# Kernel tuning notes

Measured on AMD Instinct MI355X. Metric: run time of the kernel, lower is better.

Reference implementation:

```python
import jax, jax.numpy as jnp
import numpy as np

B, T, F_DIM = 32, 512, 128
HID, OUT, KS = 256, 4, 3
PAD_LEN = 512          # round(T * (200/stage_timepoints - 1)), stage_timepoints = 100
MMD_SIGMA = 1.0
DILATIONS = (1, 2, 4)  # config.dilation_expand = 2, num_layers = 3


def setup_inputs() -> dict:
    key = jax.random.key(0)
    keys = iter(jax.random.split(key, 40))
    s = 0.05

    def lin(o, i):
        return jax.random.normal(next(keys), (o, i), jnp.float32) * s

    def vec(o):
        return jnp.zeros((o,), jnp.float32)

    inp = {
        "feature1": jax.random.normal(next(keys), (B, F_DIM, 1, T), jnp.float32),
        "feature2": jax.random.normal(next(keys), (B, F_DIM, 1, T), jnp.float32),
    }
    # cross-attention params (A and B branches)
    for tag in ("a", "b"):
        for nm in ("q", "k", "v"):
            inp["w%s_%s" % (nm, tag)] = lin(F_DIM, F_DIM)
            inp["b%s_%s" % (nm, tag)] = vec(F_DIM)
    # TCN layers
    in_ch = F_DIM
    for i in range(3):
        inp["conv_w%d" % i] = jax.random.normal(next(keys), (HID, in_ch, KS), jnp.float32) * s
        inp["conv_b%d" % i] = vec(HID)
        inp["res_w%d" % i] = lin(HID, in_ch)
        inp["res_b%d" % i] = vec(HID)
        in_ch = HID
    inp["fc_w"] = lin(OUT, HID)
    inp["fc_b"] = vec(OUT)
    return inp


def _cross_attention(A, Bseq, wq, bq, wk, bk, wv, bv):
    # A, Bseq: [B, T, F]
    Q = A @ wq.T + bq
    K = Bseq @ wk.T + bk
    V = Bseq @ wv.T + bv
    scale = 1.0 / jnp.sqrt(jnp.asarray(Q.shape[-1], Q.dtype))
    scores = jnp.einsum('btf,bsf->bts', Q, K) * scale
    w = jax.nn.softmax(scores, axis=-1)
    return jnp.einsum('bts,bsf->btf', w, V)


def _tcn_layer(x, cw, cb, rw, rb, dilation):
    # x: [B, C, T]; causal left pad then dilated conv
    pad = (KS - 1) * dilation
    xp = jnp.pad(x, ((0, 0), (0, 0), (pad, 0)))
    out = jax.lax.conv_general_dilated(
        xp, cw, window_strides=(1,), padding='VALID',
        rhs_dilation=(dilation,), dimension_numbers=('NCH', 'OIH', 'NCH'))
    out = jax.nn.relu(out + cb[None, :, None])
    res = jnp.einsum('bct,oc->bot', x, rw) + rb[None, :, None]
    return out + res


def _pairwise_dist(x, y):
    # x, y: [B, T, F] -> [B, B, T]; ||x_i - y_j||^2 per time point via norm expansion
    sx = jnp.sum(x * x, axis=-1)  # [B, T]
    sy = jnp.sum(y * y, axis=-1)  # [B, T]
    return sx[:, None, :] + sy[None, :, :] - 2.0 * jnp.einsum('itf,jtf->ijt', x, y)


def _mmd_loss(f1, f2):
    inv = 1.0 / (2.0 * MMD_SIGMA ** 2)
    K_XX = jnp.exp(-_pairwise_dist(f1, f1) * inv)
    K_YY = jnp.exp(-_pairwise_dist(f2, f2) * inv)
    K_XY = jnp.exp(-_pairwise_dist(f1, f2) * inv)
    return jnp.mean(K_XX + K_YY - 2.0 * K_XY)


def reference(feature1, feature2,
              wq_a, bq_a, wk_a, bk_a, wv_a, bv_a,
              wq_b, bq_b, wk_b, bk_b, wv_b, bv_b,
              conv_w0, conv_b0, res_w0, res_b0,
              conv_w1, conv_b1, res_w1, res_b1,
              conv_w2, conv_b2, res_w2, res_b2,
              fc_w, fc_b):
    # [B, F, 1, T] -> [B, T, F]
    f1 = jnp.transpose(feature1[:, :, 0, :], (0, 2, 1))
    f2 = jnp.transpose(feature2[:, :, 0, :], (0, 2, 1))

    f1 = _cross_attention(f2, f1, wq_a, bq_a, wk_a, bk_a, wv_a, bv_a) * f1 + f1
    f2 = _cross_attention(f1, f2, wq_b, bq_b, wk_b, bk_b, wv_b, bv_b) * f2 + f2

    # temporal-offset padding: f1 padded right, f2 padded left, then summed
    p1 = jnp.pad(f1, ((0, 0), (0, PAD_LEN), (0, 0)))
    p2 = jnp.pad(f2, ((0, 0), (PAD_LEN, 0), (0, 0)))
    x = jnp.transpose(p1 + p2, (0, 2, 1))  # [B, F, T+PAD]

    tcn_params = ((conv_w0, conv_b0, res_w0, res_b0),
                  (conv_w1, conv_b1, res_w1, res_b1),
                  (conv_w2, conv_b2, res_w2, res_b2))
    for (cw, cb, rw, rb), d in zip(tcn_params, DILATIONS):
        x = _tcn_layer(x, cw, cb, rw, rb, d)

    pooled = jnp.mean(x, axis=2)          # [B, HID]
    output = pooled @ fc_w.T + fc_b       # [B, OUT]
    loss = _mmd_loss(f1, f2)
    return output, loss
```

## Files before the change

kernel.cpp:

```cpp
#include <hip/hip_runtime.h>

#define BB 32
#define TT 512
#define FF 128
#define HID 256
#define TP 1024

typedef __attribute__((ext_vector_type(8))) short s16x8;
typedef __attribute__((ext_vector_type(8))) unsigned short u16x8;
typedef __attribute__((ext_vector_type(4))) unsigned short u16x4;
typedef __attribute__((ext_vector_type(4))) float f32x4;

static __device__ __forceinline__ unsigned short f2bf(float f) {
    unsigned u = __builtin_bit_cast(unsigned, f);
    u = (u + 0x7FFFu + ((u >> 16) & 1u)) >> 16;
    return (unsigned short)u;
}
static __device__ __forceinline__ float bf2f(unsigned short b) {
    return __builtin_bit_cast(float, ((unsigned)b) << 16);
}

__global__ __launch_bounds__(256) void t2bf_kernel(
    const float* __restrict__ src1, const float* __restrict__ src2,
    unsigned short* __restrict__ dst1, unsigned short* __restrict__ dst2)
{
    int t0 = blockIdx.x * 32, c0 = blockIdx.y * 32;
    int sel = blockIdx.z >> 5, b = blockIdx.z & 31;
    const float* src = sel ? src2 : src1;
    unsigned short* dst = sel ? dst2 : dst1;
    __shared__ float tile[32][33];
    int tid = threadIdx.x;
    for (int l = tid; l < 1024; l += 256) {
        int c = l >> 5, t = l & 31;
        tile[c][t] = src[((size_t)b * FF + c0 + c) * TT + t0 + t];
    }
    __syncthreads();
    for (int l = tid; l < 1024; l += 256) {
        int t = l >> 5, c = l & 31;
        dst[((size_t)b * TT + t0 + t) * FF + c0 + c] = f2bf(tile[c][t]);
    }
}

static __device__ __forceinline__ void tcnw_prep(
    int idx, const float* __restrict__ cw, const float* __restrict__ rw,
    unsigned short* __restrict__ out, int Cin)
{
    int p = idx / (256 * Cin);
    int rem = idx - p * 256 * Cin;
    int o = rem / Cin, c = rem - o * Cin;
    float v = (p < 3) ? cw[(o * Cin + c) * 3 + p] : rw[o * Cin + c];
    out[idx] = f2bf(v);
}

__global__ __launch_bounds__(256) void prep_all_kernel(
    const float* __restrict__ wqa, const float* __restrict__ wka,
    const float* __restrict__ wva, const float* __restrict__ wqb,
    const float* __restrict__ wkb, const float* __restrict__ wvb,
    const float* __restrict__ cw0, const float* __restrict__ rw0,
    const float* __restrict__ cw1, const float* __restrict__ rw1,
    const float* __restrict__ cw2, const float* __restrict__ rw2,
    unsigned short* __restrict__ qkvw, unsigned short* __restrict__ wb0,
    unsigned short* __restrict__ wb1, unsigned short* __restrict__ wb2)
{
    int idx = blockIdx.x * 256 + threadIdx.x;
    if (idx < 98304) {
        int p = idx >> 14, rc = idx & 16383;
        const float* srcs[6] = {wqa, wka, wva, wqb, wkb, wvb};
        float v = srcs[p][rc];
        if (p == 0 || p == 3) v *= 0.088388347648318447f;
        qkvw[idx] = f2bf(v);
    } else if (idx < 229376) {
        tcnw_prep(idx - 98304, cw0, rw0, wb0, 128);
    } else if (idx < 491520) {
        tcnw_prep(idx - 229376, cw1, rw1, wb1, 256);
    } else if (idx < 753664) {
        tcnw_prep(idx - 491520, cw2, rw2, wb2, 256);
    }
}

__global__ __launch_bounds__(256) void proj_mfma_kernel(
    const unsigned short* __restrict__ xq_src, long long xq_bs,
    const unsigned short* __restrict__ xkv_src, long long xkv_bs,
    const unsigned short* __restrict__ w3,
    const float* __restrict__ bq, const float* __restrict__ bk,
    const float* __restrict__ bv,
    unsigned short* __restrict__ Qo, unsigned short* __restrict__ Ko,
    unsigned short* __restrict__ Vt)
{
    int t0 = blockIdx.x * 32, b = blockIdx.y;
    __shared__ __align__(16) unsigned short xsq[32 * 136];
    __shared__ __align__(16) unsigned short xskv[32 * 136];
    int tid = threadIdx.x;
    int wid = tid >> 6, lane = tid & 63;
    int n = lane & 15, g = lane >> 4;
    int tsub = (wid & 1) * 16, fh = (wid >> 1) * 64;

    for (int l = tid; l < 512; l += 256) {
        int r = l >> 4, cc = l & 15;
        *(u16x8*)&xsq[r * 136 + cc * 8] =
            *(const u16x8*)&xq_src[xq_bs * b + (size_t)(t0 + r) * FF + cc * 8];
        *(u16x8*)&xskv[r * 136 + cc * 8] =
            *(const u16x8*)&xkv_src[xkv_bs * b + (size_t)(t0 + r) * FF + cc * 8];
    }
    __syncthreads();

    f32x4 acc[3][4];
#pragma unroll
    for (int p = 0; p < 3; ++p)
#pragma unroll
        for (int i = 0; i < 4; ++i) acc[p][i] = (f32x4){0.f, 0.f, 0.f, 0.f};

#pragma unroll
    for (int kk = 0; kk < 4; ++kk) {
        s16x8 bxq = *(const s16x8*)&xsq[(tsub + n) * 136 + kk * 32 + g * 8];
        s16x8 bxkv = *(const s16x8*)&xskv[(tsub + n) * 136 + kk * 32 + g * 8];
#pragma unroll
        for (int i = 0; i < 4; ++i) {
            const unsigned short* wb = &w3[(size_t)(fh + i * 16 + n) * 128 + kk * 32 + g * 8];
            s16x8 a0 = *(const s16x8*)&wb[0];
            s16x8 a1 = *(const s16x8*)&wb[16384];
            s16x8 a2 = *(const s16x8*)&wb[32768];
            acc[0][i] = __builtin_amdgcn_mfma_f32_16x16x32_bf16(a0, bxq, acc[0][i], 0, 0, 0);
            acc[1][i] = __builtin_amdgcn_mfma_f32_16x16x32_bf16(a1, bxkv, acc[1][i], 0, 0, 0);
            acc[2][i] = __builtin_amdgcn_mfma_f32_16x16x32_bf16(a2, bxkv, acc[2][i], 0, 0, 0);
        }
    }

    const float scale = 0.088388347648318447f;
    int t = t0 + tsub + n;
#pragma unroll
    for (int i = 0; i < 4; ++i) {
        int fb = fh + i * 16 + g * 4;
        u16x4 pk;
#pragma unroll
        for (int r = 0; r < 4; ++r) pk[r] = f2bf(acc[0][i][r] + bq[fb + r] * scale);
        *(u16x4*)&Qo[((size_t)b * TT + t) * FF + fb] = pk;
#pragma unroll
        for (int r = 0; r < 4; ++r) pk[r] = f2bf(acc[1][i][r] + bk[fb + r]);
        *(u16x4*)&Ko[((size_t)b * TT + t) * FF + fb] = pk;
#pragma unroll
        for (int r = 0; r < 4; ++r)
            Vt[((size_t)b * FF + fb + r) * TT + t] = f2bf(acc[2][i][r] + bv[fb + r]);
    }
}

__global__ __launch_bounds__(256) void attn_mfma_kernel(
    const unsigned short* __restrict__ Qb, const unsigned short* __restrict__ Kb,
    const unsigned short* __restrict__ Vtb,
    const float* __restrict__ orig, long long bso, int cso, int tso,
    float* __restrict__ out_tf, unsigned short* __restrict__ out_x, int xoff)
{
    __shared__ __align__(16) unsigned short Ks[64 * 136];
    __shared__ __align__(16) unsigned short Vs[128 * 72];
    __shared__ __align__(16) unsigned short Ps[4 * 16 * 68];

    int t0 = blockIdx.x * 64, b = blockIdx.y;
    int tid = threadIdx.x;
    int wid = tid >> 6, lane = tid & 63;
    int n = lane & 15, g = lane >> 4;
    int q0 = t0 + wid * 16;
    unsigned short* Pw = &Ps[wid * 1088];

    s16x8 qf[4];
#pragma unroll
    for (int kk = 0; kk < 4; ++kk)
        qf[kk] = *(const s16x8*)&Qb[((size_t)b * TT + q0 + n) * FF + kk * 32 + g * 8];

    u16x8 kst[4], vst[4];
#pragma unroll
    for (int ii = 0; ii < 4; ++ii) {
        int l = tid + 256 * ii;
        kst[ii] = *(const u16x8*)&Kb[((size_t)b * TT + (l >> 4)) * FF + (l & 15) * 8];
        vst[ii] = *(const u16x8*)&Vtb[((size_t)b * FF + (l >> 3)) * TT + (l & 7) * 8];
    }

    f32x4 O[8];
#pragma unroll
    for (int ft = 0; ft < 8; ++ft) O[ft] = (f32x4){0.f, 0.f, 0.f, 0.f};
    float m[4] = {-1e30f, -1e30f, -1e30f, -1e30f};
    float lsum[4] = {0.f, 0.f, 0.f, 0.f};

    for (int it = 0; it < 8; ++it) {
        __syncthreads();
#pragma unroll
        for (int ii = 0; ii < 4; ++ii) {
            int l = tid + 256 * ii;
            *(u16x8*)&Ks[(l >> 4) * 136 + (l & 15) * 8] = kst[ii];
            *(u16x8*)&Vs[(l >> 3) * 72 + (l & 7) * 8] = vst[ii];
        }
        __syncthreads();
        if (it < 7) {
            int s0n = (it + 1) * 64;
#pragma unroll
            for (int ii = 0; ii < 4; ++ii) {
                int l = tid + 256 * ii;
                kst[ii] = *(const u16x8*)&Kb[((size_t)b * TT + s0n + (l >> 4)) * FF + (l & 15) * 8];
                vst[ii] = *(const u16x8*)&Vtb[((size_t)b * FF + (l >> 3)) * TT + s0n + (l & 7) * 8];
            }
        }

        f32x4 acc[4];
#pragma unroll
        for (int st = 0; st < 4; ++st) acc[st] = (f32x4){0.f, 0.f, 0.f, 0.f};
#pragma unroll
        for (int kk = 0; kk < 4; ++kk) {
#pragma unroll
            for (int st = 0; st < 4; ++st) {
                s16x8 kf = *(const s16x8*)&Ks[(st * 16 + n) * 136 + kk * 32 + g * 8];
                acc[st] = __builtin_amdgcn_mfma_f32_16x16x32_bf16(qf[kk], kf, acc[st], 0, 0, 0);
            }
        }

        float mnew[4], c[4], rs[4];
#pragma unroll
        for (int r = 0; r < 4; ++r) {
            float tm = fmaxf(fmaxf(acc[0][r], acc[1][r]), fmaxf(acc[2][r], acc[3][r]));
#pragma unroll
            for (int msk = 1; msk < 16; msk <<= 1) tm = fmaxf(tm, __shfl_xor(tm, msk));
            mnew[r] = fmaxf(m[r], tm);
            c[r] = __expf(m[r] - mnew[r]);
            m[r] = mnew[r];
            rs[r] = 0.f;
        }
#pragma unroll
        for (int st = 0; st < 4; ++st) {
#pragma unroll
            for (int r = 0; r < 4; ++r) {
                float p = __expf(acc[st][r] - mnew[r]);
                rs[r] += p;
                Pw[(g * 4 + r) * 68 + st * 16 + n] = f2bf(p);
            }
        }
#pragma unroll
        for (int r = 0; r < 4; ++r) {
#pragma unroll
            for (int msk = 1; msk < 16; msk <<= 1) rs[r] += __shfl_xor(rs[r], msk);
            lsum[r] = lsum[r] * c[r] + rs[r];
        }
#pragma unroll
        for (int ft = 0; ft < 8; ++ft) {
#pragma unroll
            for (int r = 0; r < 4; ++r) O[ft][r] *= c[r];
        }

#pragma unroll
        for (int ks = 0; ks < 2; ++ks) {
            s16x8 pf = *(const s16x8*)&Pw[n * 68 + ks * 32 + g * 8];
#pragma unroll
            for (int ft = 0; ft < 8; ++ft) {
                s16x8 vf = *(const s16x8*)&Vs[(ft * 16 + n) * 72 + ks * 32 + g * 8];
                O[ft] = __builtin_amdgcn_mfma_f32_16x16x32_bf16(pf, vf, O[ft], 0, 0, 0);
            }
        }
    }

    float rinv[4];
#pragma unroll
    for (int r = 0; r < 4; ++r) rinv[r] = 1.f / lsum[r];
#pragma unroll
    for (int ft = 0; ft < 8; ++ft) {
        int f = ft * 16 + n;
#pragma unroll
        for (int r = 0; r < 4; ++r) {
            int q = q0 + g * 4 + r;
            float val = O[ft][r] * rinv[r];
            float xv = orig[bso * b + (size_t)f * cso + (size_t)q * tso];
            float res = val * xv + xv;
            out_tf[((size_t)b * TT + q) * FF + f] = res;
            out_x[((size_t)b * TP + xoff + q) * FF + f] = f2bf(res);
        }
    }
}

__global__ __launch_bounds__(256) void mmd_kernel(
    const float* __restrict__ f1, const float* __restrict__ f2,
    float* __restrict__ partials)
{
    int t = blockIdx.x;
    __shared__ float v1[32][129], v2[32][129];
    __shared__ float red[256];
    int tid = threadIdx.x;
    for (int l = tid; l < 4096; l += 256) {
        int i = l >> 7, f = l & 127;
        v1[i][f] = f1[((size_t)i * TT + t) * FF + f];
        v2[i][f] = f2[((size_t)i * TT + t) * FF + f];
    }
    __syncthreads();
    float s = 0.f;
    for (int r = 0; r < 4; ++r) {
        int p = tid + 256 * r;
        int i = p >> 5, j = p & 31;
        float dxx = 0.f, dyy = 0.f, dxy = 0.f;
        for (int f = 0; f < 128; ++f) {
            float a = v1[i][f], b_ = v1[j][f], c = v2[i][f], d = v2[j][f];
            float e1 = a - b_, e2 = c - d, e3 = a - d;
            dxx += e1 * e1; dyy += e2 * e2; dxy += e3 * e3;
        }
        s += __expf(-0.5f * dxx) + __expf(-0.5f * dyy) - 2.f * __expf(-0.5f * dxy);
    }
    red[tid] = s;
    __syncthreads();
    for (int off = 128; off; off >>= 1) {
        if (tid < off) red[tid] += red[tid + off];
        __syncthreads();
    }
    if (tid == 0) partials[t] = red[0];
}

__global__ __launch_bounds__(256, 2) void tcn_mfma_kernel(
    const unsigned short* __restrict__ x, int Cin, int d,
    const unsigned short* __restrict__ w4,
    const float* __restrict__ cb, const float* __restrict__ rb,
    unsigned short* __restrict__ out, float* __restrict__ pool_out, int do_pool)
{
    int t0 = blockIdx.x * 256, o0 = blockIdx.y * 64, b = blockIdx.z;
    __shared__ __align__(16) unsigned short xs[264 * 40];
    __shared__ __align__(16) unsigned short wsh[4 * 64 * 40];
    __shared__ float pool_s[4][64];
    int tid = threadIdx.x;
    int wid = tid >> 6, lane = tid & 63;
    int n = lane & 15, g = lane >> 4;
    int wt = wid * 64;
    int d2 = 2 * d;
    int nrow = 256 + d2;
    const unsigned short* xb = x + (size_t)b * TP * Cin;

    int gg = tid & 3;
    int xr0 = tid >> 2;
    int tg0 = t0 - d2 + xr0;
    bool xv4 = xr0 < d2;
    const unsigned short* wbase = w4 + (size_t)(o0 + (tid >> 2)) * Cin + gg * 8;
    size_t wps = (size_t)256 * Cin;

    u16x8 sx0, sx1, sx2, sx3, sx4, sw0, sw1, sw2, sw3;
    const u16x8 zz = {0, 0, 0, 0, 0, 0, 0, 0};
#define LDST(C0)                                                               \
    do {                                                                       \
        sx0 = (tg0 >= 0) ? *(const u16x8*)&xb[(size_t)tg0 * Cin + (C0) + gg * 8] : zz; \
        sx1 = *(const u16x8*)&xb[(size_t)(tg0 + 64) * Cin + (C0) + gg * 8];    \
        sx2 = *(const u16x8*)&xb[(size_t)(tg0 + 128) * Cin + (C0) + gg * 8];   \
        sx3 = *(const u16x8*)&xb[(size_t)(tg0 + 192) * Cin + (C0) + gg * 8];   \
        sx4 = xv4 ? *(const u16x8*)&xb[(size_t)(tg0 + 256) * Cin + (C0) + gg * 8] : zz; \
        sw0 = *(const u16x8*)&wbase[(C0)];                                     \
        sw1 = *(const u16x8*)&wbase[wps + (C0)];                               \
        sw2 = *(const u16x8*)&wbase[2 * wps + (C0)];                           \
        sw3 = *(const u16x8*)&wbase[3 * wps + (C0)];                           \
    } while (0)

    f32x4 accc[4][4], accr[4][4];
#pragma unroll
    for (int i = 0; i < 4; ++i)
#pragma unroll
        for (int j = 0; j < 4; ++j) {
            accc[i][j] = (f32x4){0.f, 0.f, 0.f, 0.f};
            accr[i][j] = (f32x4){0.f, 0.f, 0.f, 0.f};
        }

    LDST(0);
    for (int c0 = 0; c0 < Cin; c0 += 32) {
        __syncthreads();
        *(u16x8*)&xs[xr0 * 40 + gg * 8] = sx0;
        *(u16x8*)&xs[(xr0 + 64) * 40 + gg * 8] = sx1;
        *(u16x8*)&xs[(xr0 + 128) * 40 + gg * 8] = sx2;
        *(u16x8*)&xs[(xr0 + 192) * 40 + gg * 8] = sx3;
        if (xv4) *(u16x8*)&xs[(xr0 + 256) * 40 + gg * 8] = sx4;
        {
            int wrow = (tid >> 2) * 40 + gg * 8;
            *(u16x8*)&wsh[wrow] = sw0;
            *(u16x8*)&wsh[2560 + wrow] = sw1;
            *(u16x8*)&wsh[5120 + wrow] = sw2;
            *(u16x8*)&wsh[7680 + wrow] = sw3;
        }
        __syncthreads();
        if (c0 + 32 < Cin) LDST(c0 + 32);

        s16x8 bfr[4][3];
#pragma unroll
        for (int j = 0; j < 4; ++j) {
            int tl = wt + j * 16 + n;
#pragma unroll
            for (int k = 0; k < 3; ++k)
                bfr[j][k] = *(const s16x8*)&xs[(tl + k * d) * 40 + g * 8];
        }
#pragma unroll
        for (int i = 0; i < 4; ++i) {
            int wrow = (i * 16 + n) * 40 + g * 8;
            s16x8 a0 = *(const s16x8*)&wsh[wrow];
            s16x8 a1 = *(const s16x8*)&wsh[2560 + wrow];
            s16x8 a2 = *(const s16x8*)&wsh[5120 + wrow];
            s16x8 ar = *(const s16x8*)&wsh[7680 + wrow];
#pragma unroll
            for (int j = 0; j < 4; ++j) {
                accc[i][j] = __builtin_amdgcn_mfma_f32_16x16x32_bf16(a0, bfr[j][0], accc[i][j], 0, 0, 0);
                accc[i][j] = __builtin_amdgcn_mfma_f32_16x16x32_bf16(a1, bfr[j][1], accc[i][j], 0, 0, 0);
                accc[i][j] = __builtin_amdgcn_mfma_f32_16x16x32_bf16(a2, bfr[j][2], accc[i][j], 0, 0, 0);
                accr[i][j] = __builtin_amdgcn_mfma_f32_16x16x32_bf16(ar, bfr[j][2], accr[i][j], 0, 0, 0);
            }
        }
    }
#undef LDST

#pragma unroll
    for (int i = 0; i < 4; ++i) {
        int ob = o0 + i * 16 + g * 4;
        float cbv0 = cb[ob], cbv1 = cb[ob + 1], cbv2 = cb[ob + 2], cbv3 = cb[ob + 3];
        float rbv0 = rb[ob], rbv1 = rb[ob + 1], rbv2 = rb[ob + 2], rbv3 = rb[ob + 3];
        float ps0 = 0.f, ps1 = 0.f, ps2 = 0.f, ps3 = 0.f;
#pragma unroll
        for (int j = 0; j < 4; ++j) {
            int t = t0 + wt + j * 16 + n;
            float v0 = fmaxf(accc[i][j][0] + cbv0, 0.f) + accr[i][j][0] + rbv0;
            float v1 = fmaxf(accc[i][j][1] + cbv1, 0.f) + accr[i][j][1] + rbv1;
            float v2 = fmaxf(accc[i][j][2] + cbv2, 0.f) + accr[i][j][2] + rbv2;
            float v3 = fmaxf(accc[i][j][3] + cbv3, 0.f) + accr[i][j][3] + rbv3;
            ps0 += v0; ps1 += v1; ps2 += v2; ps3 += v3;
            if (!do_pool) {
                u16x4 pk;
                pk[0] = f2bf(v0); pk[1] = f2bf(v1); pk[2] = f2bf(v2); pk[3] = f2bf(v3);
                *(u16x4*)&out[((size_t)b * TP + t) * HID + ob] = pk;
            }
        }
        if (do_pool) {
#pragma unroll
            for (int msk = 1; msk < 16; msk <<= 1) {
                ps0 += __shfl_xor(ps0, msk);
                ps1 += __shfl_xor(ps1, msk);
                ps2 += __shfl_xor(ps2, msk);
                ps3 += __shfl_xor(ps3, msk);
            }
            if (n == 0) {
                int ol = i * 16 + g * 4;
                pool_s[wid][ol + 0] = ps0;
                pool_s[wid][ol + 1] = ps1;
                pool_s[wid][ol + 2] = ps2;
                pool_s[wid][ol + 3] = ps3;
            }
        }
    }
    if (do_pool) {
        __syncthreads();
        if (tid < 64) {
            float s = pool_s[0][tid] + pool_s[1][tid] + pool_s[2][tid] + pool_s[3][tid];
            pool_out[((size_t)b * 4 + blockIdx.x) * HID + o0 + tid] = s;
        }
    }
}

__global__ __launch_bounds__(256) void final_kernel(
    const float* __restrict__ pp, const float* __restrict__ fcw,
    const float* __restrict__ fcb, const float* __restrict__ partials,
    float* __restrict__ dout)
{
    int tid = threadIdx.x;
    if (tid < 128) {
        int b = tid >> 2, k = tid & 3;
        float s = 0.f;
        for (int c = 0; c < HID; ++c) {
            float pc = 0.f;
#pragma unroll
            for (int xs = 0; xs < 4; ++xs) pc += pp[((size_t)b * 4 + xs) * HID + c];
            s += pc * fcw[k * HID + c];
        }
        dout[tid] = fcb[k] + s * (1.f / 1024.f);
    } else if (tid < 192) {
        int lane = tid - 128;
        float s = 0.f;
        for (int j = 0; j < 8; ++j) s += partials[lane + 64 * j];
        for (int off = 32; off; off >>= 1) s += __shfl_down(s, off);
        if (lane == 0) dout[128] = s * (1.f / (32.f * 32.f * 512.f));
    }
}

extern "C" void kernel_launch(void* const* d_in, const int* in_sizes, int n_in,
                              void* d_out, int out_size, void* d_ws, size_t ws_size,
                              hipStream_t stream)
{
    const float* feat1 = (const float*)d_in[0];
    const float* feat2 = (const float*)d_in[1];
    const float* wq_a = (const float*)d_in[2];
    const float* bq_a = (const float*)d_in[3];
    const float* wk_a = (const float*)d_in[4];
    const float* bk_a = (const float*)d_in[5];
    const float* wv_a = (const float*)d_in[6];
    const float* bv_a = (const float*)d_in[7];
    const float* wq_b = (const float*)d_in[8];
    const float* bq_b = (const float*)d_in[9];
    const float* wk_b = (const float*)d_in[10];
    const float* bk_b = (const float*)d_in[11];
    const float* wv_b = (const float*)d_in[12];
    const float* bv_b = (const float*)d_in[13];
    const float* cw0 = (const float*)d_in[14];
    const float* cb0 = (const float*)d_in[15];
    const float* rw0 = (const float*)d_in[16];
    const float* rb0 = (const float*)d_in[17];
    const float* cw1 = (const float*)d_in[18];
    const float* cb1 = (const float*)d_in[19];
    const float* rw1 = (const float*)d_in[20];
    const float* rb1 = (const float*)d_in[21];
    const float* cw2 = (const float*)d_in[22];
    const float* cb2 = (const float*)d_in[23];
    const float* rw2 = (const float*)d_in[24];
    const float* rb2 = (const float*)d_in[25];
    const float* fcw = (const float*)d_in[26];
    const float* fcb = (const float*)d_in[27];
    float* dout = (float*)d_out;

    float* ws = (float*)d_ws;
    unsigned short* Qbf = (unsigned short*)ws;
    unsigned short* Kbf = (unsigned short*)(ws + 1048576);
    unsigned short* Vt  = (unsigned short*)(ws + 2097152);
    float* f1tf = ws + 3145728;
    float* f2tf = ws + 5242880;
    unsigned short* xbuf = (unsigned short*)(ws + 7340032);
    unsigned short* wbuf = (unsigned short*)(ws + 9437184);
    unsigned short* wb0 = wbuf;
    unsigned short* wb1 = wbuf + 131072;
    unsigned short* wb2 = wbuf + 393216;
    unsigned short* xbf1 = (unsigned short*)(ws + 9798144);
    unsigned short* xbf2 = (unsigned short*)(ws + 10846720);
    unsigned short* qkvw = (unsigned short*)(ws + 11895296);
    unsigned short* w3a = qkvw;
    unsigned short* w3b = qkvw + 3 * 16384;
    float* poolpart = ws + 11944448;
    float* mmdpart  = ws + 11977216;
    unsigned short* h_a = (unsigned short*)ws;
    unsigned short* h_b = (unsigned short*)(ws + 4194304);

    t2bf_kernel<<<dim3(16, 4, 64), 256, 0, stream>>>(feat1, feat2, xbf1, xbf2);
    prep_all_kernel<<<dim3(2944), 256, 0, stream>>>(
        wq_a, wk_a, wv_a, wq_b, wk_b, wv_b,
        cw0, rw0, cw1, rw1, cw2, rw2, qkvw, wb0, wb1, wb2);

    proj_mfma_kernel<<<dim3(16, 32), 256, 0, stream>>>(
        xbf2, (long long)TT * FF, xbf1, (long long)TT * FF, w3a,
        bq_a, bk_a, bv_a, Qbf, Kbf, Vt);
    attn_mfma_kernel<<<dim3(8, 32), 256, 0, stream>>>(
        Qbf, Kbf, Vt, feat1, 65536LL, 512, 1, f1tf, xbuf, 0);

    proj_mfma_kernel<<<dim3(16, 32), 256, 0, stream>>>(
        xbuf, (long long)TP * FF, xbf2, (long long)TT * FF, w3b,
        bq_b, bk_b, bv_b, Qbf, Kbf, Vt);
    attn_mfma_kernel<<<dim3(8, 32), 256, 0, stream>>>(
        Qbf, Kbf, Vt, feat2, 65536LL, 512, 1, f2tf, xbuf, 512);

    mmd_kernel<<<dim3(512), 256, 0, stream>>>(f1tf, f2tf, mmdpart);

    tcn_mfma_kernel<<<dim3(4, 4, 32), 256, 0, stream>>>(xbuf, 128, 1, wb0, cb0, rb0, h_a, nullptr, 0);
    tcn_mfma_kernel<<<dim3(4, 4, 32), 256, 0, stream>>>(h_a, 256, 2, wb1, cb1, rb1, h_b, nullptr, 0);
    tcn_mfma_kernel<<<dim3(4, 4, 32), 256, 0, stream>>>(h_b, 256, 4, wb2, cb2, rb2, h_a, poolpart, 1);

    final_kernel<<<dim3(1), 256, 0, stream>>>(poolpart, fcw, fcb, mmdpart, dout);
}
```

Measured before the change: 198.5 us.

## Fuse input transpose into projection, MFMA-based MMD Gram, attention priority hints

```diff
diff --git a/kernel.cpp b/kernel.cpp
--- a/kernel.cpp
+++ b/kernel.cpp
@@ -18,27 +18,6 @@
 }
 static __device__ __forceinline__ float bf2f(unsigned short b) {
     return __builtin_bit_cast(float, ((unsigned)b) << 16);
-}
-
-__global__ __launch_bounds__(256) void t2bf_kernel(
-    const float* __restrict__ src1, const float* __restrict__ src2,
-    unsigned short* __restrict__ dst1, unsigned short* __restrict__ dst2)
-{
-    int t0 = blockIdx.x * 32, c0 = blockIdx.y * 32;
-    int sel = blockIdx.z >> 5, b = blockIdx.z & 31;
-    const float* src = sel ? src2 : src1;
-    unsigned short* dst = sel ? dst2 : dst1;
-    __shared__ float tile[32][33];
-    int tid = threadIdx.x;
-    for (int l = tid; l < 1024; l += 256) {
-        int c = l >> 5, t = l & 31;
-        tile[c][t] = src[((size_t)b * FF + c0 + c) * TT + t0 + t];
-    }
-    __syncthreads();
-    for (int l = tid; l < 1024; l += 256) {
-        int t = l >> 5, c = l & 31;
-        dst[((size_t)b * TT + t0 + t) * FF + c0 + c] = f2bf(tile[c][t]);
-    }
 }
 
 static __device__ __forceinline__ void tcnw_prep(
@@ -79,8 +58,8 @@
 }
 
 __global__ __launch_bounds__(256) void proj_mfma_kernel(
-    const unsigned short* __restrict__ xq_src, long long xq_bs,
-    const unsigned short* __restrict__ xkv_src, long long xkv_bs,
+    const void* __restrict__ xq_src, int xq_mode, long long xq_bs,
+    const void* __restrict__ xkv_src, int xkv_mode, long long xkv_bs,
     const unsigned short* __restrict__ w3,
     const float* __restrict__ bq, const float* __restrict__ bk,
     const float* __restrict__ bv,
@@ -95,12 +74,31 @@
     int n = lane & 15, g = lane >> 4;
     int tsub = (wid & 1) * 16, fh = (wid >> 1) * 64;
 
-    for (int l = tid; l < 512; l += 256) {
-        int r = l >> 4, cc = l & 15;
-        *(u16x8*)&xsq[r * 136 + cc * 8] =
-            *(const u16x8*)&xq_src[xq_bs * b + (size_t)(t0 + r) * FF + cc * 8];
-        *(u16x8*)&xskv[r * 136 + cc * 8] =
-            *(const u16x8*)&xkv_src[xkv_bs * b + (size_t)(t0 + r) * FF + cc * 8];
+    if (xq_mode == 0) {
+        const float* s = (const float*)xq_src + (size_t)b * xq_bs;
+        for (int l = tid; l < 4096; l += 256) {
+            int c = l >> 5, tt = l & 31;
+            xsq[tt * 136 + c] = f2bf(s[(size_t)c * TT + t0 + tt]);
+        }
+    } else {
+        const unsigned short* s = (const unsigned short*)xq_src + (size_t)b * xq_bs;
+        for (int l = tid; l < 512; l += 256) {
+            int r = l >> 4, cc = l & 15;
+            *(u16x8*)&xsq[r * 136 + cc * 8] = *(const u16x8*)&s[(size_t)(t0 + r) * FF + cc * 8];
+        }
+    }
+    if (xkv_mode == 0) {
+        const float* s = (const float*)xkv_src + (size_t)b * xkv_bs;
+        for (int l = tid; l < 4096; l += 256) {
+            int c = l >> 5, tt = l & 31;
+            xskv[tt * 136 + c] = f2bf(s[(size_t)c * TT + t0 + tt]);
+        }
+    } else {
+        const unsigned short* s = (const unsigned short*)xkv_src + (size_t)b * xkv_bs;
+        for (int l = tid; l < 512; l += 256) {
+            int r = l >> 4, cc = l & 15;
+            *(u16x8*)&xskv[r * 136 + cc * 8] = *(const u16x8*)&s[(size_t)(t0 + r) * FF + cc * 8];
+        }
     }
     __syncthreads();
 
@@ -202,6 +200,7 @@
         f32x4 acc[4];
 #pragma unroll
         for (int st = 0; st < 4; ++st) acc[st] = (f32x4){0.f, 0.f, 0.f, 0.f};
+        __builtin_amdgcn_s_setprio(1);
 #pragma unroll
         for (int kk = 0; kk < 4; ++kk) {
 #pragma unroll
@@ -210,6 +209,7 @@
                 acc[st] = __builtin_amdgcn_mfma_f32_16x16x32_bf16(qf[kk], kf, acc[st], 0, 0, 0);
             }
         }
+        __builtin_amdgcn_s_setprio(0);
 
         float mnew[4], c[4], rs[4];
 #pragma unroll
@@ -243,6 +243,7 @@
             for (int r = 0; r < 4; ++r) O[ft][r] *= c[r];
         }
 
+        __builtin_amdgcn_s_setprio(1);
 #pragma unroll
         for (int ks = 0; ks < 2; ++ks) {
             s16x8 pf = *(const s16x8*)&Pw[n * 68 + ks * 32 + g * 8];
@@ -252,6 +253,7 @@
                 O[ft] = __builtin_amdgcn_mfma_f32_16x16x32_bf16(pf, vf, O[ft], 0, 0, 0);
             }
         }
+        __builtin_amdgcn_s_setprio(0);
     }
 
     float rinv[4];
@@ -277,26 +279,64 @@
     float* __restrict__ partials)
 {
     int t = blockIdx.x;
-    __shared__ float v1[32][129], v2[32][129];
+    __shared__ __align__(16) unsigned short X1h[32 * 136], X1l[32 * 136];
+    __shared__ __align__(16) unsigned short X2h[32 * 136], X2l[32 * 136];
+    __shared__ float Gs[3][32][33];
     __shared__ float red[256];
     int tid = threadIdx.x;
+
     for (int l = tid; l < 4096; l += 256) {
         int i = l >> 7, f = l & 127;
-        v1[i][f] = f1[((size_t)i * TT + t) * FF + f];
-        v2[i][f] = f2[((size_t)i * TT + t) * FF + f];
+        float v1 = f1[((size_t)i * TT + t) * FF + f];
+        float v2 = f2[((size_t)i * TT + t) * FF + f];
+        unsigned short h1 = f2bf(v1);
+        unsigned short h2 = f2bf(v2);
+        X1h[i * 136 + f] = h1;
+        X1l[i * 136 + f] = f2bf(v1 - bf2f(h1));
+        X2h[i * 136 + f] = h2;
+        X2l[i * 136 + f] = f2bf(v2 - bf2f(h2));
     }
     __syncthreads();
+
+    int wid = tid >> 6, lane = tid & 63;
+    int n = lane & 15, g = lane >> 4;
+#pragma unroll
+    for (int uu = 0; uu < 3; ++uu) {
+        int u = wid * 3 + uu;
+        int gram = u >> 2, quad = u & 3;
+        int qi = quad >> 1, qj = quad & 1;
+        const unsigned short* Ah = (gram == 1) ? X2h : X1h;
+        const unsigned short* Al = (gram == 1) ? X2l : X1l;
+        const unsigned short* Bh = (gram == 0) ? X1h : X2h;
+        const unsigned short* Bl = (gram == 0) ? X1l : X2l;
+        f32x4 acc = (f32x4){0.f, 0.f, 0.f, 0.f};
+#pragma unroll
+        for (int kk = 0; kk < 4; ++kk) {
+            int ao = (qi * 16 + n) * 136 + kk * 32 + g * 8;
+            int bo = (qj * 16 + n) * 136 + kk * 32 + g * 8;
+            s16x8 ah = *(const s16x8*)&Ah[ao];
+            s16x8 al = *(const s16x8*)&Al[ao];
+            s16x8 bh = *(const s16x8*)&Bh[bo];
+            s16x8 bl = *(const s16x8*)&Bl[bo];
+            acc = __builtin_amdgcn_mfma_f32_16x16x32_bf16(ah, bh, acc, 0, 0, 0);
+            acc = __builtin_amdgcn_mfma_f32_16x16x32_bf16(ah, bl, acc, 0, 0, 0);
+            acc = __builtin_amdgcn_mfma_f32_16x16x32_bf16(al, bh, acc, 0, 0, 0);
+        }
+#pragma unroll
+        for (int r = 0; r < 4; ++r)
+            Gs[gram][qi * 16 + g * 4 + r][qj * 16 + n] = acc[r];
+    }
+    __syncthreads();
+
     float s = 0.f;
+#pragma unroll
     for (int r = 0; r < 4; ++r) {
         int p = tid + 256 * r;
         int i = p >> 5, j = p & 31;
-        float dxx = 0.f, dyy = 0.f, dxy = 0.f;
-        for (int f = 0; f < 128; ++f) {
-            float a = v1[i][f], b_ = v1[j][f], c = v2[i][f], d = v2[j][f];
-            float e1 = a - b_, e2 = c - d, e3 = a - d;
-            dxx += e1 * e1; dyy += e2 * e2; dxy += e3 * e3;
-        }
-        s += __expf(-0.5f * dxx) + __expf(-0.5f * dyy) - 2.f * __expf(-0.5f * dxy);
+        float d11 = Gs[0][i][i] + Gs[0][j][j] - 2.f * Gs[0][i][j];
+        float d22 = Gs[1][i][i] + Gs[1][j][j] - 2.f * Gs[1][i][j];
+        float d12 = Gs[0][i][i] + Gs[1][j][j] - 2.f * Gs[2][i][j];
+        s += __expf(-0.5f * d11) + __expf(-0.5f * d22) - 2.f * __expf(-0.5f * d12);
     }
     red[tid] = s;
     __syncthreads();
@@ -516,29 +556,26 @@
     unsigned short* wb0 = wbuf;
     unsigned short* wb1 = wbuf + 131072;
     unsigned short* wb2 = wbuf + 393216;
-    unsigned short* xbf1 = (unsigned short*)(ws + 9798144);
-    unsigned short* xbf2 = (unsigned short*)(ws + 10846720);
-    unsigned short* qkvw = (unsigned short*)(ws + 11895296);
+    unsigned short* qkvw = (unsigned short*)(ws + 9764864);
     unsigned short* w3a = qkvw;
     unsigned short* w3b = qkvw + 3 * 16384;
-    float* poolpart = ws + 11944448;
-    float* mmdpart  = ws + 11977216;
+    float* poolpart = ws + 9814016;
+    float* mmdpart  = ws + 9846784;
     unsigned short* h_a = (unsigned short*)ws;
     unsigned short* h_b = (unsigned short*)(ws + 4194304);
 
-    t2bf_kernel<<<dim3(16, 4, 64), 256, 0, stream>>>(feat1, feat2, xbf1, xbf2);
     prep_all_kernel<<<dim3(2944), 256, 0, stream>>>(
         wq_a, wk_a, wv_a, wq_b, wk_b, wv_b,
         cw0, rw0, cw1, rw1, cw2, rw2, qkvw, wb0, wb1, wb2);
 
     proj_mfma_kernel<<<dim3(16, 32), 256, 0, stream>>>(
-        xbf2, (long long)TT * FF, xbf1, (long long)TT * FF, w3a,
+        feat2, 0, 65536LL, feat1, 0, 65536LL, w3a,
         bq_a, bk_a, bv_a, Qbf, Kbf, Vt);
     attn_mfma_kernel<<<dim3(8, 32), 256, 0, stream>>>(
         Qbf, Kbf, Vt, feat1, 65536LL, 512, 1, f1tf, xbuf, 0);
 
     proj_mfma_kernel<<<dim3(16, 32), 256, 0, stream>>>(
-        xbuf, (long long)TP * FF, xbf2, (long long)TT * FF, w3b,
+        xbuf, 1, (long long)TP * FF, feat2, 0, 65536LL, w3b,
         bq_b, bk_b, bv_b, Qbf, Kbf, Vt);
     attn_mfma_kernel<<<dim3(8, 32), 256, 0, stream>>>(
         Qbf, Kbf, Vt, feat2, 65536LL, 512, 1, f2tf, xbuf, 512);
```

After: 182.7 us. 8.0% less time.
